# Performance work log

Hardware: AMD Instinct MI355X
Metric: run time of the kernel (lower is better)

The kernel has to match this reference:

```python
import jax, jax.numpy as jnp
import numpy as np

N_ATOMS = 100000
N_EDGES = 6400000
CUTOFF = 12.0
CUTOFF_SR = 2.0
CUTOFF_SQ = CUTOFF * CUTOFF
KEHALF = 7.199822675975274  # ASE kehalf, unit factors = 1


def poly6_switch(d, cutoff):
    # Poly6 smooth switch-off: 1 at d=0, 0 at d>=cutoff
    x = d / cutoff
    sw = 1.0 - 10.0 * x**3 + 15.0 * x**4 - 6.0 * x**5
    return jnp.where(d < cutoff, sw, jnp.zeros_like(sw))


def setup_inputs() -> dict:
    key = jax.random.key(0)
    k1, k2, k3, k4, k5 = jax.random.split(key, 5)
    atomic_charges = jax.random.normal(k1, (N_ATOMS,), dtype=jnp.float32) * 0.3
    atomic_dipoles = jax.random.normal(k2, (N_ATOMS,), dtype=jnp.float32) * 0.1
    # distances in (0.5, 13.5): some pairs inside short-range, some beyond cutoff
    distances = jax.random.uniform(k3, (N_EDGES,), dtype=jnp.float32) * 13.0 + 0.5
    idx_i = jax.random.randint(k4, (N_EDGES,), 0, N_ATOMS, dtype=jnp.int32)
    idx_j = jax.random.randint(k5, (N_EDGES,), 0, N_ATOMS, dtype=jnp.int32)
    return {
        "atomic_charges": atomic_charges,
        "atomic_dipoles": atomic_dipoles,
        "distances": distances,
        "idx_i": idx_i,
        "idx_j": idx_j,
    }


def reference(atomic_charges, atomic_dipoles, distances, idx_i, idx_j):
    # gather per-edge charges / dipoles
    qi = atomic_charges[idx_i]
    qj = atomic_charges[idx_j]
    di = atomic_dipoles[idx_i]
    dj = atomic_dipoles[idx_j]

    d = distances
    d_sh = jnp.sqrt(d * d + 1.0)  # shielded distance

    sw_off = poly6_switch(d, CUTOFF_SR)
    sw_on = 1.0 - sw_off

    # split_distance=True branch (cutoff != cutoff_short_range):
    # shifted-force Coulomb (charge-charge, ~1/d)
    E_ord_q = 1.0 / d + d / CUTOFF_SQ - 2.0 / CUTOFF
    E_sh_q = 1.0 / d_sh + d_sh / CUTOFF_SQ - 2.0 / CUTOFF
    E_q = KEHALF * qi * qj * (sw_off * E_sh_q + sw_on * E_ord_q)

    # dipole-dipole term (~1/d^3), same shielded/ordinary blending
    E_ord_d = 1.0 / d**3
    E_sh_d = 1.0 / d_sh**3
    E_d = KEHALF * di * dj * (sw_off * E_sh_d + sw_on * E_ord_d)

    E = E_q + E_d
    E = jnp.where(d <= CUTOFF, E, jnp.zeros_like(E))

    # scatter-sum per-edge energies to atoms
    return jax.ops.segment_sum(E, idx_i, num_segments=N_ATOMS)
```

## Files before the change

### kernel.cpp

```cpp
#include <hip/hip_runtime.h>
#include <hip/hip_bf16.h>
#include <hip/hip_fp16.h>

#define CUTOFF_C    12.0f
#define CUTOFF_SR_C 2.0f
#define CUTOFF_SQ_C 144.0f
#define KEHALF_C    7.199822675975274f

__device__ __forceinline__ float edge_energy(float d, float qi, float qj,
                                             float di, float dj) {
    float inv_d   = __frcp_rn(d);
    float dsh     = __fsqrt_rn(fmaf(d, d, 1.0f));
    float inv_dsh = __frcp_rn(dsh);
    float x  = d * (1.0f / CUTOFF_SR_C);
    float x3 = x * x * x;
    float sw = fmaf(x3, fmaf(x, fmaf(x, -6.0f, 15.0f), -10.0f), 1.0f);
    float sw_off = (d < CUTOFF_SR_C) ? sw : 0.0f;
    float Eoq = inv_d   + fmaf(d,   (1.0f / CUTOFF_SQ_C), -(2.0f / CUTOFF_C));
    float Esq = inv_dsh + fmaf(dsh, (1.0f / CUTOFF_SQ_C), -(2.0f / CUTOFF_C));
    float Eq  = (KEHALF_C * qi * qj) * fmaf(sw_off, Esq - Eoq, Eoq);
    float Eod = inv_d * inv_d * inv_d;
    float Esd = inv_dsh * inv_dsh * inv_dsh;
    float Ed  = (KEHALF_C * di * dj) * fmaf(sw_off, Esd - Eod, Eod);
    return Eq + Ed;
}

__device__ __forceinline__ __half2 vw_make(float d, __half2 hqdj) {
    float2 qdj    = __half22float2(hqdj);
    float inv_d   = __frcp_rn(d);
    float dsh     = __fsqrt_rn(fmaf(d, d, 1.0f));
    float inv_dsh = __frcp_rn(dsh);
    float x  = d * (1.0f / CUTOFF_SR_C);
    float x3 = x * x * x;
    float sw = fmaf(x3, fmaf(x, fmaf(x, -6.0f, 15.0f), -10.0f), 1.0f);
    float sw_off = (d < CUTOFF_SR_C) ? sw : 0.0f;
    float Foq = inv_d   + fmaf(d,   (1.0f / CUTOFF_SQ_C), -(2.0f / CUTOFF_C));
    float Fsq = inv_dsh + fmaf(dsh, (1.0f / CUTOFF_SQ_C), -(2.0f / CUTOFF_C));
    float F   = fmaf(sw_off, Fsq - Foq, Foq);
    float God = inv_d * inv_d * inv_d;
    float Gsd = inv_dsh * inv_dsh * inv_dsh;
    float G   = fmaf(sw_off, Gsd - God, God);
    return __floats2half2_rn(KEHALF_C * qdj.x * F, KEHALF_C * qdj.y * G);
}

__device__ __forceinline__ unsigned h2bits(__half2 h) {
    union { __half2 h; unsigned u; } c; c.h = h; return c.u;
}
__device__ __forceinline__ __half2 bits2h(unsigned u) {
    union { unsigned u; __half2 h; } c; c.u = u; return c.h;
}
template <typename T>
__device__ __forceinline__ auto atom_add_h2(T* p, T v, int)
    -> decltype(atomicAdd(p, v), void()) {
    atomicAdd(p, v);
}
template <typename T>
__device__ __forceinline__ void atom_add_h2(T* p, T v, long) {
    unsigned* u = (unsigned*)p;
    unsigned old = *u, assumed;
    do {
        assumed = old;
        __half2 sum = __hadd2(bits2h(assumed), v);
        old = atomicCAS(u, assumed, h2bits(sum));
    } while (old != assumed);
}

__global__ __launch_bounds__(256) void pc_pack_qd_h(
    const float* __restrict__ q,
    const float* __restrict__ dip,
    __half2*     __restrict__ qd,
    int n_atoms)
{
    int a = blockIdx.x * 256 + threadIdx.x;
    if (a < n_atoms) qd[a] = __floats2half2_rn(q[a], dip[a]);
}

template <int CH, int BLK>
__global__ __launch_bounds__(BLK) void pc_scatter_fused(
    const float*   __restrict__ dist,
    const int*     __restrict__ idx_i,
    const int*     __restrict__ idx_j,
    const __half2* __restrict__ qd,
    __half2*       __restrict__ partial,
    int n_edges, int n4, int S, int gps, int n_atoms, int nch)
{
    extern __shared__ __half2 acc2[];

    const int c    = blockIdx.x % nch;
    const int s    = blockIdx.x / nch;
    const int base = c * CH;
    const int lim  = min(CH, n_atoms - base);

    const __half2 hzero = __floats2half2_rn(0.0f, 0.0f);
    for (int i = threadIdx.x; i < CH; i += BLK) acc2[i] = hzero;
    __syncthreads();

    const int g0 = s * gps;
    const int g1 = min(g0 + gps, n4);
    const int4*   idxi4 = (const int4*)idx_i;
    const int4*   idxj4 = (const int4*)idx_j;
    const float4* dist4 = (const float4*)dist;

    for (int g = g0 + (int)threadIdx.x; g < g1; g += BLK) {
        int4   i4 = idxi4[g];
        int4   j4 = idxj4[g];
        float4 d4 = dist4[g];

        int      ii[4] = { i4.x, i4.y, i4.z, i4.w };
        int      jj[4] = { j4.x, j4.y, j4.z, j4.w };
        float    dd[4] = { d4.x, d4.y, d4.z, d4.w };
        unsigned lc[4];
        bool     vl[4];
        __half2  qh[4];

        #pragma unroll
        for (int k = 0; k < 4; ++k) {
            lc[k] = (unsigned)(ii[k] - base);
            vl[k] = (lc[k] < (unsigned)CH) && (dd[k] <= CUTOFF_C);
        }
        #pragma unroll
        for (int k = 0; k < 4; ++k)
            qh[k] = vl[k] ? qd[jj[k]] : hzero;
        #pragma unroll
        for (int k = 0; k < 4; ++k) {
            if (vl[k]) {
                __half2 vw = vw_make(dd[k], qh[k]);
                atom_add_h2(&acc2[lc[k]], vw, 0);
            }
        }
    }

    if (s == S - 1) {
        for (int e = (n4 << 2) + (int)threadIdx.x; e < n_edges; e += BLK) {
            int i = idx_i[e];
            float d = dist[e];
            unsigned local = (unsigned)(i - base);
            if (local < (unsigned)CH && d <= CUTOFF_C) {
                __half2 vw = vw_make(d, qd[idx_j[e]]);
                atom_add_h2(&acc2[local], vw, 0);
            }
        }
    }

    __syncthreads();
    __half2* row = partial + (size_t)s * n_atoms + base;
    for (int i = threadIdx.x; i < lim; i += BLK) row[i] = acc2[i];
}

__global__ __launch_bounds__(256) void pc_reduce_vw(
    const __half2* __restrict__ partial,
    const float*   __restrict__ q,
    const float*   __restrict__ dip,
    float*         __restrict__ out,
    int n_atoms, int S)
{
    __shared__ float2 sh[256];
    int a0   = blockIdx.x * 64;
    int lane = threadIdx.x & 63;
    int w    = threadIdx.x >> 6;
    int a    = a0 + lane;

    float sv = 0.0f, sw = 0.0f;
    if (a < n_atoms) {
        int per = S >> 2;
        const __half2* p = partial + a;
        int s = w * per, send = s + per;
        for (; s < send; ++s) {
            float2 t = __half22float2(p[(size_t)s * n_atoms]);
            sv += t.x; sw += t.y;
        }
    }
    sh[threadIdx.x] = make_float2(sv, sw);
    __syncthreads();
    if (w == 0 && a < n_atoms) {
        float2 t0 = sh[lane],       t1 = sh[64 + lane];
        float2 t2 = sh[128 + lane], t3 = sh[192 + lane];
        float fv = (t0.x + t1.x) + (t2.x + t3.x);
        float fw = (t0.y + t1.y) + (t2.y + t3.y);
        out[a] = fmaf(q[a], fv, dip[a] * fw);
    }
}

__global__ __launch_bounds__(256) void pc_dipole_edges_atomic(
    const float* __restrict__ q,
    const float* __restrict__ dip,
    const float* __restrict__ dist,
    const int*   __restrict__ idx_i,
    const int*   __restrict__ idx_j,
    float*       __restrict__ out,
    int n_edges)
{
    int t = blockIdx.x * blockDim.x + threadIdx.x;
    const int stride = gridDim.x * blockDim.x;
    for (int e = t; e < n_edges; e += stride) {
        float d = dist[e];
        if (d > CUTOFF_C) continue;
        int i = idx_i[e], j = idx_j[e];
        atomicAdd(&out[i], edge_energy(d, q[i], q[j], dip[i], dip[j]));
    }
}

#define CH_T0 33792
#define CH_T1 20480

static bool probe_lds(const void* f, int blk, size_t lds) {
    hipError_t e1 = hipFuncSetAttribute(
        f, hipFuncAttributeMaxDynamicSharedMemorySize, (int)lds);
    int nb = 0;
    hipError_t e2 = hipOccupancyMaxActiveBlocksPerMultiprocessor(&nb, f, blk, lds);
    return (e1 == hipSuccess && e2 == hipSuccess && nb >= 1);
}

extern "C" void kernel_launch(void* const* d_in, const int* in_sizes, int n_in,
                              void* d_out, int out_size, void* d_ws, size_t ws_size,
                              hipStream_t stream) {
    const float* q     = (const float*)d_in[0];
    const float* dip   = (const float*)d_in[1];
    const float* dist  = (const float*)d_in[2];
    const int*   idx_i = (const int*)d_in[3];
    const int*   idx_j = (const int*)d_in[4];
    float*       out   = (float*)d_out;

    int n_edges = in_sizes[2];
    int n_atoms = out_size;
    int n4      = n_edges >> 2;

    int tier, CH, BLK, S;
    size_t lds;
    if (probe_lds((const void*)&pc_scatter_fused<CH_T0, 1024>, 1024,
                  (size_t)CH_T0 * 4)) {
        tier = 0; CH = CH_T0; BLK = 1024; S = 84; lds = (size_t)CH_T0 * 4;
    } else {
        tier = 1; CH = CH_T1; BLK = 512;  S = 48; lds = (size_t)CH_T1 * 4;
    }
    int nch = (n_atoms + CH - 1) / CH;

    size_t qd_b  = ((size_t)n_atoms * sizeof(__half2) + 255) & ~(size_t)255;
    size_t avail = (ws_size > qd_b) ? ws_size - qd_b : 0;
    int S_fit = (int)(avail / ((size_t)n_atoms * sizeof(__half2)));
    if (S_fit < S) S = S_fit & ~3;

    if (S >= 8 && n_atoms > 0) {
        __half2* qd      = (__half2*)d_ws;
        __half2* partial = (__half2*)((char*)d_ws + qd_b);
        int      gps     = (n4 + S - 1) / S;

        pc_pack_qd_h<<<(n_atoms + 255) / 256, 256, 0, stream>>>(q, dip, qd,
                                                                n_atoms);
        if (tier == 0)
            pc_scatter_fused<CH_T0, 1024><<<S * nch, 1024, lds, stream>>>(
                dist, idx_i, idx_j, qd, partial, n_edges, n4, S, gps,
                n_atoms, nch);
        else
            pc_scatter_fused<CH_T1, 512><<<S * nch, 512, lds, stream>>>(
                dist, idx_i, idx_j, qd, partial, n_edges, n4, S, gps,
                n_atoms, nch);
        pc_reduce_vw<<<(n_atoms + 63) / 64, 256, 0, stream>>>(
            partial, q, dip, out, n_atoms, S);
    } else {
        hipMemsetAsync(out, 0, (size_t)n_atoms * sizeof(float), stream);
        int grid = (n_edges + 255) / 256;
        pc_dipole_edges_atomic<<<grid, 256, 0, stream>>>(
            q, dip, dist, idx_i, idx_j, out, n_edges);
    }
}
```

Before: 165.8 us.

## Split scatter into producer pass writing per-edge half2 weights plus consumer passes

The fused scatter used to re-read idx_j, the distances and the gathered qd for every atom chunk. Now a first kernel computes the per-edge packed half2 weights once, writes them to a workspace buffer, and accumulates chunk 0. Later kernels read only idx_i and the packed weights for the remaining chunks, skipping zero entries. This removes the repeated random gathers and the repeated weight arithmetic, at the cost of an extra edge-sized write and read, a different split count per chunk, and a more complex reduce.

```diff
diff --git a/kernel.cpp b/kernel.cpp
--- a/kernel.cpp
+++ b/kernel.cpp
@@ -6,6 +6,11 @@
 #define CUTOFF_SR_C 2.0f
 #define CUTOFF_SQ_C 144.0f
 #define KEHALF_C    7.199822675975274f
+
+#define CH_T0  33792
+#define S1_N   252
+#define BLK1   1024
+#define BLK2   1024
 
 __device__ __forceinline__ float edge_energy(float d, float qi, float qj,
                                              float di, float dj) {
@@ -75,24 +80,21 @@
     if (a < n_atoms) qd[a] = __floats2half2_rn(q[a], dip[a]);
 }
 
-template <int CH, int BLK>
-__global__ __launch_bounds__(BLK) void pc_scatter_fused(
+template <int CH>
+__global__ __launch_bounds__(BLK1) void pc_produce_scatter0(
     const float*   __restrict__ dist,
     const int*     __restrict__ idx_i,
     const int*     __restrict__ idx_j,
     const __half2* __restrict__ qd,
-    __half2*       __restrict__ partial,
-    int n_edges, int n4, int S, int gps, int n_atoms, int nch)
+    __half2*       __restrict__ vw,
+    __half2*       __restrict__ partial0,
+    int n_edges, int n4, int S1, int gps)
 {
     extern __shared__ __half2 acc2[];
 
-    const int c    = blockIdx.x % nch;
-    const int s    = blockIdx.x / nch;
-    const int base = c * CH;
-    const int lim  = min(CH, n_atoms - base);
-
+    const int s = blockIdx.x;
     const __half2 hzero = __floats2half2_rn(0.0f, 0.0f);
-    for (int i = threadIdx.x; i < CH; i += BLK) acc2[i] = hzero;
+    for (int i = threadIdx.x; i < CH; i += BLK1) acc2[i] = hzero;
     __syncthreads();
 
     const int g0 = s * gps;
@@ -101,58 +103,113 @@
     const int4*   idxj4 = (const int4*)idx_j;
     const float4* dist4 = (const float4*)dist;
 
-    for (int g = g0 + (int)threadIdx.x; g < g1; g += BLK) {
-        int4   i4 = idxi4[g];
+    for (int g = g0 + (int)threadIdx.x; g < g1; g += BLK1) {
         int4   j4 = idxj4[g];
         float4 d4 = dist4[g];
-
+        int4   i4 = idxi4[g];
+
+        int   jj[4] = { j4.x, j4.y, j4.z, j4.w };
+        int   ii[4] = { i4.x, i4.y, i4.z, i4.w };
+        float dd[4] = { d4.x, d4.y, d4.z, d4.w };
+        bool  sv[4];
+        __half2 qh[4];
+
+        #pragma unroll
+        for (int k = 0; k < 4; ++k) sv[k] = (dd[k] <= CUTOFF_C);
+        #pragma unroll
+        for (int k = 0; k < 4; ++k) qh[k] = sv[k] ? qd[jj[k]] : hzero;
+
+        __half2 vwv[4];
+        #pragma unroll
+        for (int k = 0; k < 4; ++k)
+            vwv[k] = sv[k] ? vw_make(dd[k], qh[k]) : hzero;
+
+        uint4 st;
+        st.x = h2bits(vwv[0]); st.y = h2bits(vwv[1]);
+        st.z = h2bits(vwv[2]); st.w = h2bits(vwv[3]);
+        ((uint4*)vw)[g] = st;
+
+        #pragma unroll
+        for (int k = 0; k < 4; ++k) {
+            unsigned lc = (unsigned)ii[k];
+            if (sv[k] && lc < (unsigned)CH)
+                atom_add_h2(&acc2[lc], vwv[k], 0);
+        }
+    }
+
+    if (s == S1 - 1) {
+        for (int e = (n4 << 2) + (int)threadIdx.x; e < n_edges; e += BLK1) {
+            float d = dist[e];
+            __half2 r = hzero;
+            if (d <= CUTOFF_C) r = vw_make(d, qd[idx_j[e]]);
+            vw[e] = r;
+            unsigned lc = (unsigned)idx_i[e];
+            if (d <= CUTOFF_C && lc < (unsigned)CH)
+                atom_add_h2(&acc2[lc], r, 0);
+        }
+    }
+
+    __syncthreads();
+    __half2* row = partial0 + (size_t)s * CH;
+    for (int i = threadIdx.x; i < CH; i += BLK1) row[i] = acc2[i];
+}
+
+template <int CH>
+__global__ __launch_bounds__(BLK2) void pc_scatter_rest(
+    const int*     __restrict__ idx_i,
+    const __half2* __restrict__ vw,
+    __half2*       __restrict__ partial12,
+    int n_edges, int n4, int S2, int gps, int nrest)
+{
+    extern __shared__ __half2 acc2[];
+
+    const int cr   = blockIdx.x % nrest;
+    const int s    = blockIdx.x / nrest;
+    const int base = (cr + 1) * CH;
+
+    const __half2 hzero = __floats2half2_rn(0.0f, 0.0f);
+    for (int i = threadIdx.x; i < CH; i += BLK2) acc2[i] = hzero;
+    __syncthreads();
+
+    const int g0 = s * gps;
+    const int g1 = min(g0 + gps, n4);
+    const int4*  idxi4 = (const int4*)idx_i;
+    const uint4* vw4   = (const uint4*)vw;
+
+    for (int g = g0 + (int)threadIdx.x; g < g1; g += BLK2) {
+        int4  i4 = idxi4[g];
+        uint4 u4 = vw4[g];
         int      ii[4] = { i4.x, i4.y, i4.z, i4.w };
-        int      jj[4] = { j4.x, j4.y, j4.z, j4.w };
-        float    dd[4] = { d4.x, d4.y, d4.z, d4.w };
-        unsigned lc[4];
-        bool     vl[4];
-        __half2  qh[4];
-
+        unsigned uu[4] = { u4.x, u4.y, u4.z, u4.w };
         #pragma unroll
         for (int k = 0; k < 4; ++k) {
-            lc[k] = (unsigned)(ii[k] - base);
-            vl[k] = (lc[k] < (unsigned)CH) && (dd[k] <= CUTOFF_C);
-        }
-        #pragma unroll
-        for (int k = 0; k < 4; ++k)
-            qh[k] = vl[k] ? qd[jj[k]] : hzero;
-        #pragma unroll
-        for (int k = 0; k < 4; ++k) {
-            if (vl[k]) {
-                __half2 vw = vw_make(dd[k], qh[k]);
-                atom_add_h2(&acc2[lc[k]], vw, 0);
-            }
-        }
-    }
-
-    if (s == S - 1) {
-        for (int e = (n4 << 2) + (int)threadIdx.x; e < n_edges; e += BLK) {
-            int i = idx_i[e];
-            float d = dist[e];
-            unsigned local = (unsigned)(i - base);
-            if (local < (unsigned)CH && d <= CUTOFF_C) {
-                __half2 vw = vw_make(d, qd[idx_j[e]]);
-                atom_add_h2(&acc2[local], vw, 0);
-            }
-        }
-    }
-
-    __syncthreads();
-    __half2* row = partial + (size_t)s * n_atoms + base;
-    for (int i = threadIdx.x; i < lim; i += BLK) row[i] = acc2[i];
-}
-
-__global__ __launch_bounds__(256) void pc_reduce_vw(
-    const __half2* __restrict__ partial,
+            unsigned lc = (unsigned)(ii[k] - base);
+            if (lc < (unsigned)CH && uu[k] != 0u)
+                atom_add_h2(&acc2[lc], bits2h(uu[k]), 0);
+        }
+    }
+
+    if (s == S2 - 1) {
+        for (int e = (n4 << 2) + (int)threadIdx.x; e < n_edges; e += BLK2) {
+            unsigned lc = (unsigned)(idx_i[e] - base);
+            __half2 r = vw[e];
+            if (lc < (unsigned)CH && h2bits(r) != 0u)
+                atom_add_h2(&acc2[lc], r, 0);
+        }
+    }
+
+    __syncthreads();
+    __half2* row = partial12 + ((size_t)cr * S2 + s) * CH;
+    for (int i = threadIdx.x; i < CH; i += BLK2) row[i] = acc2[i];
+}
+
+__global__ __launch_bounds__(256) void pc_reduce_vw2(
+    const __half2* __restrict__ partial0,
+    const __half2* __restrict__ partial12,
     const float*   __restrict__ q,
     const float*   __restrict__ dip,
     float*         __restrict__ out,
-    int n_atoms, int S)
+    int n_atoms, int CH, int S1, int S2)
 {
     __shared__ float2 sh[256];
     int a0   = blockIdx.x * 64;
@@ -162,11 +219,18 @@
 
     float sv = 0.0f, sw = 0.0f;
     if (a < n_atoms) {
+        int c = a / CH;
+        const __half2* p;
+        int S, col;
+        if (c == 0) { p = partial0; S = S1; col = a; }
+        else {
+            p = partial12 + (size_t)(c - 1) * S2 * CH;
+            S = S2; col = a - c * CH;
+        }
         int per = S >> 2;
-        const __half2* p = partial + a;
         int s = w * per, send = s + per;
         for (; s < send; ++s) {
-            float2 t = __half22float2(p[(size_t)s * n_atoms]);
+            float2 t = __half22float2(p[(size_t)s * CH + col]);
             sv += t.x; sw += t.y;
         }
     }
@@ -199,9 +263,6 @@
         atomicAdd(&out[i], edge_energy(d, q[i], q[j], dip[i], dip[j]));
     }
 }
-
-#define CH_T0 33792
-#define CH_T1 20480
 
 static bool probe_lds(const void* f, int blk, size_t lds) {
     hipError_t e1 = hipFuncSetAttribute(
@@ -225,38 +286,46 @@
     int n_atoms = out_size;
     int n4      = n_edges >> 2;
 
-    int tier, CH, BLK, S;
-    size_t lds;
-    if (probe_lds((const void*)&pc_scatter_fused<CH_T0, 1024>, 1024,
-                  (size_t)CH_T0 * 4)) {
-        tier = 0; CH = CH_T0; BLK = 1024; S = 84; lds = (size_t)CH_T0 * 4;
-    } else {
-        tier = 1; CH = CH_T1; BLK = 512;  S = 48; lds = (size_t)CH_T1 * 4;
-    }
-    int nch = (n_atoms + CH - 1) / CH;
+    const int CH  = CH_T0;
+    size_t    lds = (size_t)CH * sizeof(__half2);
+
+    int nch   = (n_atoms + CH - 1) / CH;
+    int nrest = nch - 1;
+    int S2    = 0;
+    if (nrest > 0) {
+        S2 = (256 / nrest) & ~3;
+        if (S2 < 4) S2 = 4;
+    }
+
+    bool ok1 = probe_lds((const void*)&pc_produce_scatter0<CH_T0>, BLK1, lds);
+    bool ok2 = (nrest == 0) ||
+               probe_lds((const void*)&pc_scatter_rest<CH_T0>, BLK2, lds);
 
     size_t qd_b  = ((size_t)n_atoms * sizeof(__half2) + 255) & ~(size_t)255;
-    size_t avail = (ws_size > qd_b) ? ws_size - qd_b : 0;
-    int S_fit = (int)(avail / ((size_t)n_atoms * sizeof(__half2)));
-    if (S_fit < S) S = S_fit & ~3;
-
-    if (S >= 8 && n_atoms > 0) {
-        __half2* qd      = (__half2*)d_ws;
-        __half2* partial = (__half2*)((char*)d_ws + qd_b);
-        int      gps     = (n4 + S - 1) / S;
+    size_t vw_b  = ((size_t)n_edges * sizeof(__half2) + 255) & ~(size_t)255;
+    size_t p0_b  = ((size_t)S1_N * CH * sizeof(__half2) + 255) & ~(size_t)255;
+    size_t p12_b = (size_t)nrest * S2 * CH * sizeof(__half2);
+    size_t need  = qd_b + vw_b + p0_b + p12_b;
+
+    if (ok1 && ok2 && need <= ws_size && n_atoms > 0) {
+        __half2* qd  = (__half2*)d_ws;
+        __half2* vw  = (__half2*)((char*)d_ws + qd_b);
+        __half2* p0  = (__half2*)((char*)d_ws + qd_b + vw_b);
+        __half2* p12 = (__half2*)((char*)d_ws + qd_b + vw_b + p0_b);
+
+        int gps1 = (n4 + S1_N - 1) / S1_N;
 
         pc_pack_qd_h<<<(n_atoms + 255) / 256, 256, 0, stream>>>(q, dip, qd,
                                                                 n_atoms);
-        if (tier == 0)
-            pc_scatter_fused<CH_T0, 1024><<<S * nch, 1024, lds, stream>>>(
-                dist, idx_i, idx_j, qd, partial, n_edges, n4, S, gps,
-                n_atoms, nch);
-        else
-            pc_scatter_fused<CH_T1, 512><<<S * nch, 512, lds, stream>>>(
-                dist, idx_i, idx_j, qd, partial, n_edges, n4, S, gps,
-                n_atoms, nch);
-        pc_reduce_vw<<<(n_atoms + 63) / 64, 256, 0, stream>>>(
-            partial, q, dip, out, n_atoms, S);
+        pc_produce_scatter0<CH_T0><<<S1_N, BLK1, lds, stream>>>(
+            dist, idx_i, idx_j, qd, vw, p0, n_edges, n4, S1_N, gps1);
+        if (nrest > 0) {
+            int gps2 = (n4 + S2 - 1) / S2;
+            pc_scatter_rest<CH_T0><<<S2 * nrest, BLK2, lds, stream>>>(
+                idx_i, vw, p12, n_edges, n4, S2, gps2, nrest);
+        }
+        pc_reduce_vw2<<<(n_atoms + 63) / 64, 256, 0, stream>>>(
+            p0, p12, q, dip, out, n_atoms, CH, S1_N, S2);
     } else {
         hipMemsetAsync(out, 0, (size_t)n_atoms * sizeof(float), stream);
         int grid = (n_edges + 255) / 256;
```

Result: slower. 192.7 us (+16.2%).

## Replace per-edge Coulomb/dipole math with LDS lookup table and linear interpolation

Applied to the files above, without the earlier changes.

Adds a scatter kernel variant that builds a 2049-entry table of the distance-only factors F and G in shared memory per block. Each edge then does two table reads and a linear interpolation instead of a reciprocal, a sqrt and the switch polynomial. Block indexing is reordered so partitions of the same chunk are adjacent, and S is now derived from the chunk count (256/nch rounded down to a multiple of 8) instead of being fixed at 84. This trades transcendental ALU work for extra LDS traffic and approximation error. Each block also pays the table-building cost.

```diff
diff --git a/kernel.cpp b/kernel.cpp
--- a/kernel.cpp
+++ b/kernel.cpp
@@ -6,6 +6,10 @@
 #define CUTOFF_SR_C 2.0f
 #define CUTOFF_SQ_C 144.0f
 #define KEHALF_C    7.199822675975274f
+
+#define CH_T0  33792
+#define LUTN   2048
+#define BLK1   1024
 
 __device__ __forceinline__ float edge_energy(float d, float qi, float qj,
                                              float di, float dj) {
@@ -25,11 +29,10 @@
     return Eq + Ed;
 }
 
-__device__ __forceinline__ __half2 vw_make(float d, __half2 hqdj) {
-    float2 qdj    = __half22float2(hqdj);
-    float inv_d   = __frcp_rn(d);
-    float dsh     = __fsqrt_rn(fmaf(d, d, 1.0f));
-    float inv_dsh = __frcp_rn(dsh);
+__device__ __forceinline__ float2 fg_exact(float d) {
+    float inv_d   = 1.0f / d;
+    float dsh     = sqrtf(fmaf(d, d, 1.0f));
+    float inv_dsh = 1.0f / dsh;
     float x  = d * (1.0f / CUTOFF_SR_C);
     float x3 = x * x * x;
     float sw = fmaf(x3, fmaf(x, fmaf(x, -6.0f, 15.0f), -10.0f), 1.0f);
@@ -40,7 +43,13 @@
     float God = inv_d * inv_d * inv_d;
     float Gsd = inv_dsh * inv_dsh * inv_dsh;
     float G   = fmaf(sw_off, Gsd - God, God);
-    return __floats2half2_rn(KEHALF_C * qdj.x * F, KEHALF_C * qdj.y * G);
+    return make_float2(KEHALF_C * F, KEHALF_C * G);
+}
+
+__device__ __forceinline__ __half2 vw_make_exact(float d, __half2 hqdj) {
+    float2 qdj = __half22float2(hqdj);
+    float2 fg  = fg_exact(d);
+    return __floats2half2_rn(qdj.x * fg.x, qdj.y * fg.y);
 }
 
 __device__ __forceinline__ unsigned h2bits(__half2 h) {
@@ -76,6 +85,96 @@
 }
 
 template <int CH, int BLK>
+__global__ __launch_bounds__(BLK) void pc_scatter_lut(
+    const float*   __restrict__ dist,
+    const int*     __restrict__ idx_i,
+    const int*     __restrict__ idx_j,
+    const __half2* __restrict__ qd,
+    __half2*       __restrict__ partial,
+    int n_edges, int n4, int S, int gps, int n_atoms, int nch)
+{
+    extern __shared__ char smem[];
+    __half2* acc2 = (__half2*)smem;
+    float2*  lut  = (float2*)(smem + (size_t)CH * sizeof(__half2));
+
+    const int s    = blockIdx.x % S;
+    const int c    = blockIdx.x / S;
+    const int base = c * CH;
+    const int lim  = min(CH, n_atoms - base);
+
+    const __half2 hzero = __floats2half2_rn(0.0f, 0.0f);
+    for (int i = threadIdx.x; i < CH; i += BLK) acc2[i] = hzero;
+
+    const float hstep = CUTOFF_C / (float)LUTN;
+    for (int k = threadIdx.x; k <= LUTN; k += BLK) {
+        float d = fmaxf((float)k * hstep, 0.25f * hstep);
+        lut[k] = fg_exact(d);
+    }
+    __syncthreads();
+
+    const int g0 = s * gps;
+    const int g1 = min(g0 + gps, n4);
+    const int4*   idxi4 = (const int4*)idx_i;
+    const int4*   idxj4 = (const int4*)idx_j;
+    const float4* dist4 = (const float4*)dist;
+    const float   dscale = (float)LUTN / CUTOFF_C;
+
+    for (int g = g0 + (int)threadIdx.x; g < g1; g += BLK) {
+        int4   i4 = idxi4[g];
+        int4   j4 = idxj4[g];
+        float4 d4 = dist4[g];
+
+        int      ii[4] = { i4.x, i4.y, i4.z, i4.w };
+        int      jj[4] = { j4.x, j4.y, j4.z, j4.w };
+        float    dd[4] = { d4.x, d4.y, d4.z, d4.w };
+        unsigned lc[4];
+        bool     vl[4];
+        __half2  qh[4];
+
+        #pragma unroll
+        for (int k = 0; k < 4; ++k) {
+            lc[k] = (unsigned)(ii[k] - base);
+            vl[k] = (lc[k] < (unsigned)CH) && (dd[k] <= CUTOFF_C);
+        }
+        #pragma unroll
+        for (int k = 0; k < 4; ++k)
+            qh[k] = vl[k] ? qd[jj[k]] : hzero;
+
+        #pragma unroll
+        for (int k = 0; k < 4; ++k) {
+            if (vl[k]) {
+                float t  = dd[k] * dscale;
+                int   kk = min((int)t, LUTN - 1);
+                float fr = t - (float)kk;
+                float2 l0 = lut[kk];
+                float2 l1 = lut[kk + 1];
+                float F = fmaf(fr, l1.x - l0.x, l0.x);
+                float G = fmaf(fr, l1.y - l0.y, l0.y);
+                float2 qdj = __half22float2(qh[k]);
+                __half2 vw = __floats2half2_rn(qdj.x * F, qdj.y * G);
+                atom_add_h2(&acc2[lc[k]], vw, 0);
+            }
+        }
+    }
+
+    if (s == S - 1) {
+        for (int e = (n4 << 2) + (int)threadIdx.x; e < n_edges; e += BLK) {
+            int i = idx_i[e];
+            float d = dist[e];
+            unsigned local = (unsigned)(i - base);
+            if (local < (unsigned)CH && d <= CUTOFF_C) {
+                __half2 vw = vw_make_exact(d, qd[idx_j[e]]);
+                atom_add_h2(&acc2[local], vw, 0);
+            }
+        }
+    }
+
+    __syncthreads();
+    __half2* row = partial + (size_t)s * n_atoms + base;
+    for (int i = threadIdx.x; i < lim; i += BLK) row[i] = acc2[i];
+}
+
+template <int CH, int BLK>
 __global__ __launch_bounds__(BLK) void pc_scatter_fused(
     const float*   __restrict__ dist,
     const int*     __restrict__ idx_i,
@@ -84,15 +183,15 @@
     __half2*       __restrict__ partial,
     int n_edges, int n4, int S, int gps, int n_atoms, int nch)
 {
-    extern __shared__ __half2 acc2[];
-
-    const int c    = blockIdx.x % nch;
-    const int s    = blockIdx.x / nch;
+    extern __shared__ __half2 accf[];
+
+    const int s    = blockIdx.x % S;
+    const int c    = blockIdx.x / S;
     const int base = c * CH;
     const int lim  = min(CH, n_atoms - base);
 
     const __half2 hzero = __floats2half2_rn(0.0f, 0.0f);
-    for (int i = threadIdx.x; i < CH; i += BLK) acc2[i] = hzero;
+    for (int i = threadIdx.x; i < CH; i += BLK) accf[i] = hzero;
     __syncthreads();
 
     const int g0 = s * gps;
@@ -105,14 +204,12 @@
         int4   i4 = idxi4[g];
         int4   j4 = idxj4[g];
         float4 d4 = dist4[g];
-
         int      ii[4] = { i4.x, i4.y, i4.z, i4.w };
         int      jj[4] = { j4.x, j4.y, j4.z, j4.w };
         float    dd[4] = { d4.x, d4.y, d4.z, d4.w };
         unsigned lc[4];
         bool     vl[4];
         __half2  qh[4];
-
         #pragma unroll
         for (int k = 0; k < 4; ++k) {
             lc[k] = (unsigned)(ii[k] - base);
@@ -123,10 +220,8 @@
             qh[k] = vl[k] ? qd[jj[k]] : hzero;
         #pragma unroll
         for (int k = 0; k < 4; ++k) {
-            if (vl[k]) {
-                __half2 vw = vw_make(dd[k], qh[k]);
-                atom_add_h2(&acc2[lc[k]], vw, 0);
-            }
+            if (vl[k])
+                atom_add_h2(&accf[lc[k]], vw_make_exact(dd[k], qh[k]), 0);
         }
     }
 
@@ -135,16 +230,14 @@
             int i = idx_i[e];
             float d = dist[e];
             unsigned local = (unsigned)(i - base);
-            if (local < (unsigned)CH && d <= CUTOFF_C) {
-                __half2 vw = vw_make(d, qd[idx_j[e]]);
-                atom_add_h2(&acc2[local], vw, 0);
-            }
+            if (local < (unsigned)CH && d <= CUTOFF_C)
+                atom_add_h2(&accf[local], vw_make_exact(d, qd[idx_j[e]]), 0);
         }
     }
 
     __syncthreads();
     __half2* row = partial + (size_t)s * n_atoms + base;
-    for (int i = threadIdx.x; i < lim; i += BLK) row[i] = acc2[i];
+    for (int i = threadIdx.x; i < lim; i += BLK) row[i] = accf[i];
 }
 
 __global__ __launch_bounds__(256) void pc_reduce_vw(
@@ -199,9 +292,6 @@
         atomicAdd(&out[i], edge_energy(d, q[i], q[j], dip[i], dip[j]));
     }
 }
-
-#define CH_T0 33792
-#define CH_T1 20480
 
 static bool probe_lds(const void* f, int blk, size_t lds) {
     hipError_t e1 = hipFuncSetAttribute(
@@ -225,34 +315,40 @@
     int n_atoms = out_size;
     int n4      = n_edges >> 2;
 
-    int tier, CH, BLK, S;
-    size_t lds;
-    if (probe_lds((const void*)&pc_scatter_fused<CH_T0, 1024>, 1024,
-                  (size_t)CH_T0 * 4)) {
-        tier = 0; CH = CH_T0; BLK = 1024; S = 84; lds = (size_t)CH_T0 * 4;
-    } else {
-        tier = 1; CH = CH_T1; BLK = 512;  S = 48; lds = (size_t)CH_T1 * 4;
-    }
+    const int CH = CH_T0;
     int nch = (n_atoms + CH - 1) / CH;
+
+    int S = (256 / nch) & ~7;
+    if (S < 8) S = 8;
+
+    size_t lds_lut = (size_t)CH * sizeof(__half2)
+                   + (size_t)(LUTN + 1) * sizeof(float2);
+    size_t lds_fus = (size_t)CH * sizeof(__half2);
+
+    bool ok_lut = probe_lds((const void*)&pc_scatter_lut<CH_T0, BLK1>,
+                            BLK1, lds_lut);
+    bool ok_fus = ok_lut ||
+                  probe_lds((const void*)&pc_scatter_fused<CH_T0, BLK1>,
+                            BLK1, lds_fus);
 
     size_t qd_b  = ((size_t)n_atoms * sizeof(__half2) + 255) & ~(size_t)255;
     size_t avail = (ws_size > qd_b) ? ws_size - qd_b : 0;
     int S_fit = (int)(avail / ((size_t)n_atoms * sizeof(__half2)));
-    if (S_fit < S) S = S_fit & ~3;
-
-    if (S >= 8 && n_atoms > 0) {
+    if (S_fit < S) S = S_fit & ~7;
+
+    if ((ok_lut || ok_fus) && S >= 8 && n_atoms > 0) {
         __half2* qd      = (__half2*)d_ws;
         __half2* partial = (__half2*)((char*)d_ws + qd_b);
         int      gps     = (n4 + S - 1) / S;
 
         pc_pack_qd_h<<<(n_atoms + 255) / 256, 256, 0, stream>>>(q, dip, qd,
                                                                 n_atoms);
-        if (tier == 0)
-            pc_scatter_fused<CH_T0, 1024><<<S * nch, 1024, lds, stream>>>(
+        if (ok_lut)
+            pc_scatter_lut<CH_T0, BLK1><<<S * nch, BLK1, lds_lut, stream>>>(
                 dist, idx_i, idx_j, qd, partial, n_edges, n4, S, gps,
                 n_atoms, nch);
         else
-            pc_scatter_fused<CH_T1, 512><<<S * nch, 512, lds, stream>>>(
+            pc_scatter_fused<CH_T0, BLK1><<<S * nch, BLK1, lds_fus, stream>>>(
                 dist, idx_i, idx_j, qd, partial, n_edges, n4, S, gps,
                 n_atoms, nch);
         pc_reduce_vw<<<(n_atoms + 63) / 64, 256, 0, stream>>>(
```

Result: no change. 164.9 us (-0.6%).

## Replace per-edge energy math with LDS lookup table and retune chunking

Applied to the files above, without the earlier changes.

The per-edge distance functions F(d) and G(d) are now read from a linear-interpolation lookup table built in LDS at block start, replacing the per-edge reciprocal, sqrt and polynomial evaluation. The launch configuration is also reworked: a smaller atom chunk with a smaller table is used when two 1024-thread blocks fit per CU, S is derived from a block budget, and the block index order changes so that consecutive blocks share a chunk. This is meant to cut ALU work in the scatter loop. In exchange it adds LDS traffic and possible bank conflicts from table reads, and interpolation error that grows near small d where 1/d^3 is steep.

```diff
diff --git a/kernel.cpp b/kernel.cpp
--- a/kernel.cpp
+++ b/kernel.cpp
@@ -6,6 +6,13 @@
 #define CUTOFF_SR_C 2.0f
 #define CUTOFF_SQ_C 144.0f
 #define KEHALF_C    7.199822675975274f
+
+#define BLK1   1024
+
+#define CH_DUO   17408
+#define LUT_DUO  1024
+#define CH_SOLO  33792
+#define LUT_SOLO 2048
 
 __device__ __forceinline__ float edge_energy(float d, float qi, float qj,
                                              float di, float dj) {
@@ -25,11 +32,10 @@
     return Eq + Ed;
 }
 
-__device__ __forceinline__ __half2 vw_make(float d, __half2 hqdj) {
-    float2 qdj    = __half22float2(hqdj);
-    float inv_d   = __frcp_rn(d);
-    float dsh     = __fsqrt_rn(fmaf(d, d, 1.0f));
-    float inv_dsh = __frcp_rn(dsh);
+__device__ __forceinline__ float2 fg_exact(float d) {
+    float inv_d   = 1.0f / d;
+    float dsh     = sqrtf(fmaf(d, d, 1.0f));
+    float inv_dsh = 1.0f / dsh;
     float x  = d * (1.0f / CUTOFF_SR_C);
     float x3 = x * x * x;
     float sw = fmaf(x3, fmaf(x, fmaf(x, -6.0f, 15.0f), -10.0f), 1.0f);
@@ -40,7 +46,13 @@
     float God = inv_d * inv_d * inv_d;
     float Gsd = inv_dsh * inv_dsh * inv_dsh;
     float G   = fmaf(sw_off, Gsd - God, God);
-    return __floats2half2_rn(KEHALF_C * qdj.x * F, KEHALF_C * qdj.y * G);
+    return make_float2(KEHALF_C * F, KEHALF_C * G);
+}
+
+__device__ __forceinline__ __half2 vw_make_exact(float d, __half2 hqdj) {
+    float2 qdj = __half22float2(hqdj);
+    float2 fg  = fg_exact(d);
+    return __floats2half2_rn(qdj.x * fg.x, qdj.y * fg.y);
 }
 
 __device__ __forceinline__ unsigned h2bits(__half2 h) {
@@ -75,8 +87,8 @@
     if (a < n_atoms) qd[a] = __floats2half2_rn(q[a], dip[a]);
 }
 
-template <int CH, int BLK>
-__global__ __launch_bounds__(BLK) void pc_scatter_fused(
+template <int CH, int LUTN, int BLK>
+__global__ __launch_bounds__(BLK) void pc_scatter_lut(
     const float*   __restrict__ dist,
     const int*     __restrict__ idx_i,
     const int*     __restrict__ idx_j,
@@ -84,15 +96,23 @@
     __half2*       __restrict__ partial,
     int n_edges, int n4, int S, int gps, int n_atoms, int nch)
 {
-    extern __shared__ __half2 acc2[];
-
-    const int c    = blockIdx.x % nch;
-    const int s    = blockIdx.x / nch;
+    extern __shared__ char smem[];
+    __half2* acc2 = (__half2*)smem;
+    float2*  lut  = (float2*)(smem + (size_t)CH * sizeof(__half2));
+
+    const int s    = blockIdx.x % S;
+    const int c    = blockIdx.x / S;
     const int base = c * CH;
     const int lim  = min(CH, n_atoms - base);
 
     const __half2 hzero = __floats2half2_rn(0.0f, 0.0f);
     for (int i = threadIdx.x; i < CH; i += BLK) acc2[i] = hzero;
+
+    const float hstep = CUTOFF_C / (float)LUTN;
+    for (int k = threadIdx.x; k <= LUTN; k += BLK) {
+        float d = fmaxf((float)k * hstep, 0.25f * hstep);
+        lut[k] = fg_exact(d);
+    }
     __syncthreads();
 
     const int g0 = s * gps;
@@ -100,6 +120,7 @@
     const int4*   idxi4 = (const int4*)idx_i;
     const int4*   idxj4 = (const int4*)idx_j;
     const float4* dist4 = (const float4*)dist;
+    const float   dscale = (float)LUTN / CUTOFF_C;
 
     for (int g = g0 + (int)threadIdx.x; g < g1; g += BLK) {
         int4   i4 = idxi4[g];
@@ -121,10 +142,19 @@
         #pragma unroll
         for (int k = 0; k < 4; ++k)
             qh[k] = vl[k] ? qd[jj[k]] : hzero;
+
         #pragma unroll
         for (int k = 0; k < 4; ++k) {
             if (vl[k]) {
-                __half2 vw = vw_make(dd[k], qh[k]);
+                float t  = dd[k] * dscale;
+                int   kk = min((int)t, LUTN - 1);
+                float fr = t - (float)kk;
+                float2 l0 = lut[kk];
+                float2 l1 = lut[kk + 1];
+                float F = fmaf(fr, l1.x - l0.x, l0.x);
+                float G = fmaf(fr, l1.y - l0.y, l0.y);
+                float2 qdj = __half22float2(qh[k]);
+                __half2 vw = __floats2half2_rn(qdj.x * F, qdj.y * G);
                 atom_add_h2(&acc2[lc[k]], vw, 0);
             }
         }
@@ -136,7 +166,7 @@
             float d = dist[e];
             unsigned local = (unsigned)(i - base);
             if (local < (unsigned)CH && d <= CUTOFF_C) {
-                __half2 vw = vw_make(d, qd[idx_j[e]]);
+                __half2 vw = vw_make_exact(d, qd[idx_j[e]]);
                 atom_add_h2(&acc2[local], vw, 0);
             }
         }
@@ -200,15 +230,13 @@
     }
 }
 
-#define CH_T0 33792
-#define CH_T1 20480
-
-static bool probe_lds(const void* f, int blk, size_t lds) {
+static int probe_blocks(const void* f, int blk, size_t lds) {
     hipError_t e1 = hipFuncSetAttribute(
         f, hipFuncAttributeMaxDynamicSharedMemorySize, (int)lds);
     int nb = 0;
     hipError_t e2 = hipOccupancyMaxActiveBlocksPerMultiprocessor(&nb, f, blk, lds);
-    return (e1 == hipSuccess && e2 == hipSuccess && nb >= 1);
+    if (e1 != hipSuccess || e2 != hipSuccess) return 0;
+    return nb;
 }
 
 extern "C" void kernel_launch(void* const* d_in, const int* in_sizes, int n_in,
@@ -225,36 +253,55 @@
     int n_atoms = out_size;
     int n4      = n_edges >> 2;
 
-    int tier, CH, BLK, S;
+    size_t lds_duo  = (size_t)CH_DUO  * sizeof(__half2)
+                    + (size_t)(LUT_DUO  + 1) * sizeof(float2);
+    size_t lds_solo = (size_t)CH_SOLO * sizeof(__half2)
+                    + (size_t)(LUT_SOLO + 1) * sizeof(float2);
+
+    int nb_duo = probe_blocks((const void*)&pc_scatter_lut<CH_DUO, LUT_DUO, BLK1>,
+                              BLK1, lds_duo);
+    int nb_solo = probe_blocks((const void*)&pc_scatter_lut<CH_SOLO, LUT_SOLO, BLK1>,
+                               BLK1, lds_solo);
+
+    bool use_duo = (nb_duo >= 2);
+    int  CH, nch, S, cap;
     size_t lds;
-    if (probe_lds((const void*)&pc_scatter_fused<CH_T0, 1024>, 1024,
-                  (size_t)CH_T0 * 4)) {
-        tier = 0; CH = CH_T0; BLK = 1024; S = 84; lds = (size_t)CH_T0 * 4;
+    if (use_duo) {
+        CH  = CH_DUO;  lds = lds_duo;
+        nch = (n_atoms + CH - 1) / CH;
+        cap = 512;
     } else {
-        tier = 1; CH = CH_T1; BLK = 512;  S = 48; lds = (size_t)CH_T1 * 4;
-    }
-    int nch = (n_atoms + CH - 1) / CH;
+        CH  = CH_SOLO; lds = lds_solo;
+        nch = (n_atoms + CH - 1) / CH;
+        cap = 256;
+    }
+    S = (cap / nch) & ~7;
+    if (S < 8) S = 8;
 
     size_t qd_b  = ((size_t)n_atoms * sizeof(__half2) + 255) & ~(size_t)255;
     size_t avail = (ws_size > qd_b) ? ws_size - qd_b : 0;
     int S_fit = (int)(avail / ((size_t)n_atoms * sizeof(__half2)));
-    if (S_fit < S) S = S_fit & ~3;
-
-    if (S >= 8 && n_atoms > 0) {
+    if (S_fit < S) S = S_fit & ~7;
+
+    bool ok = (use_duo || nb_solo >= 1) && S >= 8 && n_atoms > 0;
+
+    if (ok) {
         __half2* qd      = (__half2*)d_ws;
         __half2* partial = (__half2*)((char*)d_ws + qd_b);
         int      gps     = (n4 + S - 1) / S;
 
         pc_pack_qd_h<<<(n_atoms + 255) / 256, 256, 0, stream>>>(q, dip, qd,
                                                                 n_atoms);
-        if (tier == 0)
-            pc_scatter_fused<CH_T0, 1024><<<S * nch, 1024, lds, stream>>>(
-                dist, idx_i, idx_j, qd, partial, n_edges, n4, S, gps,
-                n_atoms, nch);
+        if (use_duo)
+            pc_scatter_lut<CH_DUO, LUT_DUO, BLK1>
+                <<<S * nch, BLK1, lds, stream>>>(
+                    dist, idx_i, idx_j, qd, partial, n_edges, n4, S, gps,
+                    n_atoms, nch);
         else
-            pc_scatter_fused<CH_T1, 512><<<S * nch, 512, lds, stream>>>(
-                dist, idx_i, idx_j, qd, partial, n_edges, n4, S, gps,
-                n_atoms, nch);
+            pc_scatter_lut<CH_SOLO, LUT_SOLO, BLK1>
+                <<<S * nch, BLK1, lds, stream>>>(
+                    dist, idx_i, idx_j, qd, partial, n_edges, n4, S, gps,
+                    n_atoms, nch);
         pc_reduce_vw<<<(n_atoms + 63) / 64, 256, 0, stream>>>(
             partial, q, dip, out, n_atoms, S);
     } else {
```

New measurement: 163.1 us. About the same (-1.6%).
